# Optimization experiments

Hardware: AMD Instinct MI355X
Metric: run time of the kernel (lower is better)

## Reference

```python
import jax, jax.numpy as jnp
import numpy as np

SEQ_LEN = 512; PATCH = 16; STRIDE = 8; D_MODEL = 768; N_HEAD = 12; N_LAYERS = 6
POOL = 1000; TOP_K = 4; PRED_LEN = 96; TREND_W = 24; SEAS = 24
PATCH_NUM = (SEQ_LEN - PATCH) // STRIDE + 2  # 64, incl. the replication-padded patch
B = 64; M = 7


def _ln(x, g, b, eps=1e-5):
    mu = jnp.mean(x, axis=-1, keepdims=True)
    v = jnp.var(x, axis=-1, keepdims=True)
    return (x - mu) * jax.lax.rsqrt(v + eps) * g + b


def _decompose(x):
    # x: [N, L]. pandas: rolling(TREND_W, center=True).mean() + bfill/ffill,
    # then seasonal = groupby(index % SEAS).transform('mean') of detrended.
    N, L = x.shape
    w = TREND_W
    right = (w - 1) // 2          # pandas centered window: [i - (w-1-right), i + right]
    left = w - 1 - right
    cs = jnp.concatenate([jnp.zeros((N, 1), x.dtype), jnp.cumsum(x, axis=1)], axis=1)
    valid = (cs[:, w:] - cs[:, :-w]) / w                      # [N, L-w+1]
    trend = jnp.concatenate([jnp.repeat(valid[:, :1], left, axis=1), valid,
                             jnp.repeat(valid[:, -1:], right, axis=1)], axis=1)
    det = x - trend
    ids = jnp.arange(L) % SEAS
    onehot = jax.nn.one_hot(ids, SEAS, dtype=x.dtype)         # [L, S]
    gmean = (det @ onehot) / jnp.sum(onehot, axis=0)          # [N, S]
    seasonal = gmean[:, ids]
    resid = x - trend - seasonal
    return jnp.stack([trend, seasonal, resid], axis=1)        # [N, 3, L]


def _gpt2(h, wpe, layer_params, lnf_g, lnf_b):
    Bh, T, D = h.shape
    h = h + wpe[:T]
    mask = jnp.tril(jnp.ones((T, T), bool))
    hd = D // N_HEAD

    def block(h, p):
        ln1g, ln1b, qkvw, qkvb, aw, ab, ln2g, ln2b, fcw, fcb, pw, pb = p
        a = _ln(h, ln1g, ln1b)
        qkv = a @ qkvw + qkvb
        q, k, v = jnp.split(qkv, 3, axis=-1)
        sh = lambda t: t.reshape(Bh, T, N_HEAD, hd).transpose(0, 2, 1, 3)
        q, k, v = sh(q), sh(k), sh(v)
        s = jnp.einsum('bhqd,bhkd->bhqk', q, k) / jnp.sqrt(jnp.asarray(hd, h.dtype))
        s = jnp.where(mask, s, jnp.asarray(-1e9, h.dtype))
        att = jax.nn.softmax(s, axis=-1)
        o = jnp.einsum('bhqk,bhkd->bhqd', att, v).transpose(0, 2, 1, 3).reshape(Bh, T, D)
        h = h + o @ aw + ab
        m = _ln(h, ln2g, ln2b)
        h = h + jax.nn.gelu(m @ fcw + fcb, approximate=True) @ pw + pb
        return h, None

    h, _ = jax.lax.scan(block, h, layer_params)
    return _ln(h, lnf_g, lnf_b)


def setup_inputs() -> dict:
    key = jax.random.key(0)
    ks = jax.random.split(key, 10)
    D = D_MODEL; F = 4 * D
    f32 = jnp.float32
    return dict(
        x=jax.random.normal(ks[0], (B, SEQ_LEN, M), f32),
        itr=1,
        in_w=jax.random.normal(ks[1], (3 * PATCH, D), f32) * 0.02,
        in_b=jnp.zeros((D,), f32),
        prompt_key=jax.random.uniform(ks[2], (POOL, D), f32, -1.0, 1.0),
        wpe=jax.random.normal(ks[3], (1024, D), f32) * 0.02,
        ln1_g=jnp.ones((N_LAYERS, D), f32), ln1_b=jnp.zeros((N_LAYERS, D), f32),
        qkv_w=jax.random.normal(ks[4], (N_LAYERS, D, 3 * D), f32) * 0.02,
        qkv_b=jnp.zeros((N_LAYERS, 3 * D), f32),
        aproj_w=jax.random.normal(ks[5], (N_LAYERS, D, D), f32) * 0.02,
        aproj_b=jnp.zeros((N_LAYERS, D), f32),
        ln2_g=jnp.ones((N_LAYERS, D), f32), ln2_b=jnp.zeros((N_LAYERS, D), f32),
        fc_w=jax.random.normal(ks[6], (N_LAYERS, D, F), f32) * 0.02,
        fc_b=jnp.zeros((N_LAYERS, F), f32),
        mproj_w=jax.random.normal(ks[7], (N_LAYERS, F, D), f32) * 0.02,
        mproj_b=jnp.zeros((N_LAYERS, D), f32),
        lnf_g=jnp.ones((D,), f32), lnf_b=jnp.zeros((D,), f32),
        out_w=jax.random.normal(ks[8], ((D // 3) * (PATCH_NUM + TOP_K), PRED_LEN), f32) * 0.02,
        out_b=jnp.zeros((PRED_LEN,), f32),
    )


def reference(x, itr, in_w, in_b, prompt_key, wpe, ln1_g, ln1_b, qkv_w, qkv_b,
              aproj_w, aproj_b, ln2_g, ln2_b, fc_w, fc_b, mproj_w, mproj_b,
              lnf_g, lnf_b, out_w, out_b):
    B_, L, M_ = x.shape
    means = jax.lax.stop_gradient(jnp.mean(x, axis=1, keepdims=True))     # detached
    xc = x - means
    stdev = jax.lax.stop_gradient(jnp.sqrt(jnp.var(xc, axis=1, keepdims=True) + 1e-5))
    xn = xc / stdev
    xr = jnp.transpose(xn, (0, 2, 1)).reshape(B_ * M_, L)                  # 'b l m -> (b m) l'
    dec = jax.lax.stop_gradient(_decompose(xr))                            # torch detaches via numpy round-trip
    # ReplicationPad1d((0, STRIDE)) then unfold(size=PATCH, step=STRIDE)
    xpad = jnp.concatenate([dec, jnp.repeat(dec[:, :, -1:], STRIDE, axis=2)], axis=2)
    starts = jnp.arange(PATCH_NUM) * STRIDE
    patches = xpad[:, :, starts[:, None] + jnp.arange(PATCH)[None, :]]     # [BM, 3, N, P]
    tok = jnp.transpose(patches, (0, 2, 1, 3)).reshape(B_ * M_, PATCH_NUM, 3 * PATCH)
    emb = tok @ in_w + in_b                                                # [BM, N, D]
    # prompt-pool retrieval (L2P-style, length=1, prompts = normalized keys)
    l2n = lambda t: t * jax.lax.rsqrt(jnp.maximum(jnp.sum(t * t, -1, keepdims=True), 1e-12))
    key_n = l2n(prompt_key)                                                # [POOL, D]
    xq = l2n(jnp.mean(emb, axis=1))                                        # [BM, D]
    sim = xq @ key_n.T                                                     # [BM, POOL]
    _, idx = jax.lax.top_k(sim, TOP_K)
    bp = key_n[idx]                                                        # [BM, K, D]
    reduce_sim = jnp.sum(bp * xq[:, None, :]) / emb.shape[0]
    prompted = jnp.concatenate([bp, emb], axis=1)                          # [BM, K+N, D]
    layer_params = (ln1_g, ln1_b, qkv_w, qkv_b, aproj_w, aproj_b,
                    ln2_g, ln2_b, fc_w, fc_b, mproj_w, mproj_b)
    h = _gpt2(prompted, wpe, layer_params, lnf_g, lnf_b)                   # [BM, K+N, D]
    o = h.reshape(B_ * M_ * 3, -1) @ out_w + out_b                         # [BM*3, PRED_LEN]
    o = o.reshape(B_, M_, 3, PRED_LEN).sum(axis=2)                         # [B, M, H]
    out = jnp.transpose(o, (0, 2, 1)) * stdev + means                      # [B, H, M]
    return out, reduce_sim
```

## Files before the change

### kernel.cpp

```cpp
#include <hip/hip_runtime.h>
#include <math.h>

#define NTOK 30464
#define NEMB 28672
typedef unsigned short ushort;
typedef __attribute__((ext_vector_type(8))) __bf16 bf16x8_t;
typedef __attribute__((ext_vector_type(4))) float f32x4_t;

#if defined(__has_builtin)
#if __has_builtin(__builtin_amdgcn_global_load_lds)
#define HAS_GLL 1
#endif
#endif

__device__ __forceinline__ ushort f2bf(float f) {
  unsigned int u = __float_as_uint(f);
  u += 0x7fffu + ((u >> 16) & 1u);
  return (ushort)(u >> 16);
}
__device__ __forceinline__ float bf2f(ushort u) {
  return __uint_as_float(((unsigned int)u) << 16);
}

#ifdef HAS_GLL
__device__ __forceinline__ void gll16(const ushort* g, ushort* l) {
  __builtin_amdgcn_global_load_lds(
      (const __attribute__((address_space(1))) unsigned int*)g,
      (__attribute__((address_space(3))) unsigned int*)l, 16, 0, 0);
}
#endif

__device__ __forceinline__ float block_reduce_sum(float v, float* scratch) {
  __syncthreads();
  #pragma unroll
  for (int o = 32; o; o >>= 1) v += __shfl_xor(v, o, 64);
  int wid = threadIdx.x >> 6, lane = threadIdx.x & 63;
  if (lane == 0) scratch[wid] = v;
  __syncthreads();
  if (threadIdx.x == 0) {
    float s = 0.f;
    int nw = (blockDim.x + 63) >> 6;
    for (int i = 0; i < nw; i++) s += scratch[i];
    scratch[0] = s;
  }
  __syncthreads();
  return scratch[0];
}

__device__ __forceinline__ float gelu_f(float x) {
  float z2 = 1.5957691216057308f * (x + 0.044715f * x * x * x);
  return x / (1.0f + __expf(-z2));
}

__global__ __launch_bounds__(256) void revin_kernel(const float* __restrict__ x,
    float* __restrict__ xr, float* __restrict__ means, float* __restrict__ stdev) {
  int bm = blockIdx.x;
  int b = bm / 7, m = bm % 7;
  int tid = threadIdx.x;
  __shared__ float red[8];
  float v0 = x[(size_t)b * 3584 + (size_t)tid * 7 + m];
  float v1 = x[(size_t)b * 3584 + (size_t)(tid + 256) * 7 + m];
  float s  = block_reduce_sum(v0 + v1, red);
  float ss = block_reduce_sum(v0 * v0 + v1 * v1, red);
  float mean = s * (1.0f / 512.0f);
  float var  = ss * (1.0f / 512.0f) - mean * mean;
  float sd = sqrtf(var + 1e-5f);
  if (tid == 0) { means[bm] = mean; stdev[bm] = sd; }
  float inv = 1.0f / sd;
  xr[(size_t)bm * 512 + tid]       = (v0 - mean) * inv;
  xr[(size_t)bm * 512 + tid + 256] = (v1 - mean) * inv;
}

__global__ __launch_bounds__(256) void decompose_kernel(const float* __restrict__ xr,
    float* __restrict__ dec) {
  int n = blockIdx.x, tid = threadIdx.x;
  __shared__ float xv[512];
  __shared__ float tr[512];
  __shared__ float sumS[24];
  for (int l = tid; l < 512; l += 256) xv[l] = xr[(size_t)n * 512 + l];
  if (tid < 24) sumS[tid] = 0.f;
  __syncthreads();
  for (int l = tid; l < 512; l += 256) {
    int t0 = l - 12; t0 = t0 < 0 ? 0 : (t0 > 488 ? 488 : t0);
    float s = 0.f;
    #pragma unroll
    for (int j = 0; j < 24; j++) s += xv[t0 + j];
    float t = s * (1.0f / 24.0f);
    tr[l] = t;
    atomicAdd(&sumS[l % 24], xv[l] - t);
  }
  __syncthreads();
  if (tid < 24) sumS[tid] *= (tid < 8) ? (1.0f / 22.0f) : (1.0f / 21.0f);
  __syncthreads();
  float* dp = dec + (size_t)n * 1536;
  for (int l = tid; l < 512; l += 256) {
    float t = tr[l], se = sumS[l % 24];
    dp[l] = t;
    dp[512 + l] = se;
    dp[1024 + l] = xv[l] - t - se;
  }
}

__global__ __launch_bounds__(256) void embed_kernel(const float* __restrict__ dec,
    const float* __restrict__ in_w, const float* __restrict__ in_b, float* __restrict__ h) {
  int blk = blockIdx.x;
  int n = blk >> 2, pg = blk & 3;
  int tid = threadIdx.x;
  __shared__ __align__(16) float tok[16][48];
  for (int idx = tid; idx < 768; idx += 256) {
    int p = idx / 48, k = idx - p * 48;
    int c = k >> 4, j = k & 15;
    int l = (pg * 16 + p) * 8 + j; if (l > 511) l = 511;
    tok[p][k] = dec[(size_t)n * 1536 + (size_t)c * 512 + l];
  }
  __syncthreads();
  const int d0 = tid, d1 = tid + 256, d2 = tid + 512;
  float acc[16][3];
  float b0 = in_b[d0], b1 = in_b[d1], b2 = in_b[d2];
  #pragma unroll
  for (int p = 0; p < 16; p++) { acc[p][0] = b0; acc[p][1] = b1; acc[p][2] = b2; }
  for (int kq = 0; kq < 12; kq++) {
    float w0[4], w1[4], w2[4];
    #pragma unroll
    for (int kk = 0; kk < 4; kk++) {
      const float* wp = in_w + (size_t)(kq * 4 + kk) * 768;
      w0[kk] = wp[d0]; w1[kk] = wp[d1]; w2[kk] = wp[d2];
    }
    #pragma unroll
    for (int p = 0; p < 16; p++) {
      float4 t = *(const float4*)&tok[p][kq * 4];
      acc[p][0] += t.x * w0[0]; acc[p][1] += t.x * w1[0]; acc[p][2] += t.x * w2[0];
      acc[p][0] += t.y * w0[1]; acc[p][1] += t.y * w1[1]; acc[p][2] += t.y * w2[1];
      acc[p][0] += t.z * w0[2]; acc[p][1] += t.z * w1[2]; acc[p][2] += t.z * w2[2];
      acc[p][0] += t.w * w0[3]; acc[p][1] += t.w * w1[3]; acc[p][2] += t.w * w2[3];
    }
  }
  #pragma unroll
  for (int p = 0; p < 16; p++) {
    float* outp = h + ((size_t)n * 68 + 4 + pg * 16 + p) * 768;
    outp[d0] = acc[p][0]; outp[d1] = acc[p][1]; outp[d2] = acc[p][2];
  }
}

__global__ __launch_bounds__(256) void keyn_kernel(const float* __restrict__ pkey,
    float* __restrict__ keyn, double* __restrict__ kinv) {
  int k = blockIdx.x, tid = threadIdx.x;
  __shared__ double redd[4];
  float v[3];
  double ss = 0.0;
  #pragma unroll
  for (int i = 0; i < 3; i++) {
    v[i] = pkey[(size_t)k * 768 + tid + i * 256];
    ss += (double)v[i] * (double)v[i];
  }
  #pragma unroll
  for (int o = 32; o; o >>= 1) ss += __shfl_xor(ss, o, 64);
  int wid = tid >> 6, lane = tid & 63;
  if (lane == 0) redd[wid] = ss;
  __syncthreads();
  if (tid == 0) redd[0] = redd[0] + redd[1] + redd[2] + redd[3];
  __syncthreads();
  ss = redd[0];
  double inv = 1.0 / sqrt(ss > 1e-12 ? ss : 1e-12);
  #pragma unroll
  for (int i = 0; i < 3; i++)
    keyn[(size_t)k * 768 + tid + i * 256] = (float)((double)v[i] * inv);
  if (tid == 0) kinv[k] = inv;
}

__global__ __launch_bounds__(256) void xq_kernel(const float* __restrict__ h,
    float* __restrict__ xq) {
  int n = blockIdx.x, tid = threadIdx.x;
  __shared__ float red[8];
  float vals[3];
  float ssl = 0.f;
  #pragma unroll
  for (int i = 0; i < 3; i++) {
    int d = tid + i * 256;
    const float* p = h + ((size_t)n * 68 + 4) * 768 + d;
    float s = 0.f;
    for (int pc = 0; pc < 64; pc++) s += p[(size_t)pc * 768];
    s *= (1.0f / 64.0f);
    vals[i] = s; ssl += s * s;
  }
  float ss = block_reduce_sum(ssl, red);
  float inv = rsqrtf(fmaxf(ss, 1e-12f));
  #pragma unroll
  for (int i = 0; i < 3; i++)
    xq[(size_t)n * 768 + tid + i * 256] = vals[i] * inv;
}

__global__ void zero_kernel(float* p) {
  if (threadIdx.x == 0 && blockIdx.x == 0) p[0] = 0.f;
}

__global__ __launch_bounds__(256) void sim_kernel(
    const float* __restrict__ xq, const float* __restrict__ pkey,
    const double* __restrict__ kinv, double* __restrict__ simd) {
  int n = blockIdx.y;
  int kbase = blockIdx.x * 128;
  int tid = threadIdx.x;
  __shared__ __align__(16) float xqv[768];
  #pragma unroll
  for (int i = 0; i < 3; i++) xqv[tid + i * 256] = xq[(size_t)n * 768 + tid + i * 256];
  __syncthreads();
  int lane = tid & 63, wid = tid >> 6;
  double xd[12];
  #pragma unroll
  for (int i = 0; i < 12; i++) xd[i] = (double)xqv[lane * 12 + i];

  for (int k4 = kbase + wid * 4; k4 < kbase + 128; k4 += 16) {
    int kt[4];
    #pragma unroll
    for (int t = 0; t < 4; t++) { int k = k4 + t; kt[t] = k < 1000 ? k : 999; }
    float4 v[4][3];
    #pragma unroll
    for (int t = 0; t < 4; t++)
      #pragma unroll
      for (int j = 0; j < 3; j++)
        v[t][j] = *(const float4*)(pkey + (size_t)kt[t] * 768 + lane * 12 + j * 4);
    double a[4] = {0.0, 0.0, 0.0, 0.0};
    #pragma unroll
    for (int t = 0; t < 4; t++)
      #pragma unroll
      for (int j = 0; j < 3; j++) {
        a[t] += (double)v[t][j].x * xd[4 * j + 0];
        a[t] += (double)v[t][j].y * xd[4 * j + 1];
        a[t] += (double)v[t][j].z * xd[4 * j + 2];
        a[t] += (double)v[t][j].w * xd[4 * j + 3];
      }
    #pragma unroll
    for (int t = 0; t < 4; t++)
      #pragma unroll
      for (int o = 32; o; o >>= 1) a[t] += __shfl_xor(a[t], o, 64);
    if (lane == 0) {
      #pragma unroll
      for (int t = 0; t < 4; t++) {
        int k = k4 + t;
        if (k < 1000) simd[(size_t)n * 1000 + k] = a[t] * kinv[k];
      }
    }
  }
}

__global__ __launch_bounds__(256) void topk_kernel(
    const float* __restrict__ xq, const double* __restrict__ simd_g,
    const float* __restrict__ keyn, const float* __restrict__ wpe,
    float* __restrict__ h, float* __restrict__ rs_out) {
  int n = blockIdx.x, tid = threadIdx.x;
  __shared__ __align__(16) float xqv[768];
  __shared__ double simd_s[1000];
  __shared__ int idxs[4];
  __shared__ double redv[4];
  __shared__ int redi[4];
  __shared__ float red2[8];
  #pragma unroll
  for (int i = 0; i < 3; i++) xqv[tid + i * 256] = xq[(size_t)n * 768 + tid + i * 256];
  for (int k = tid; k < 1000; k += 256) simd_s[k] = simd_g[(size_t)n * 1000 + k];
  __syncthreads();
  int lane = tid & 63, wid = tid >> 6;
  for (int r = 0; r < 4; r++) {
    double bv = -1e300; int bi = 0x7fffffff;
    for (int k = tid; k < 1000; k += 256) {
      double v = simd_s[k];
      if (v > bv || (v == bv && k < bi)) { bv = v; bi = k; }
    }
    #pragma unroll
    for (int off = 32; off; off >>= 1) {
      double ov = __shfl_xor(bv, off, 64);
      int oi = __shfl_xor(bi, off, 64);
      if (ov > bv || (ov == bv && oi < bi)) { bv = ov; bi = oi; }
    }
    if (lane == 0) { redv[wid] = bv; redi[wid] = bi; }
    __syncthreads();
    if (tid == 0) {
      double fv = redv[0]; int fi = redi[0];
      for (int w = 1; w < 4; w++)
        if (redv[w] > fv || (redv[w] == fv && redi[w] < fi)) { fv = redv[w]; fi = redi[w]; }
      idxs[r] = fi; simd_s[fi] = -1e300;
    }
    __syncthreads();
  }
  float part = 0.f;
  for (int r = 0; r < 4; r++) {
    int ki = idxs[r];
    const float* kp = keyn + (size_t)ki * 768;
    const float* wp = wpe + (size_t)r * 768;
    float* hp = h + ((size_t)n * 68 + r) * 768;
    #pragma unroll
    for (int i = 0; i < 3; i++) {
      int d = tid + i * 256;
      float kv = kp[d];
      hp[d] = kv + wp[d];
      part += kv * xqv[d];
    }
  }
  part = block_reduce_sum(part, red2);
  if (tid == 0) atomicAdd(rs_out, part * (1.0f / 448.0f));
}

__global__ __launch_bounds__(256) void addwpe_kernel(const float* __restrict__ wpe,
    float* __restrict__ h) {
  int np = blockIdx.x;
  int n = np >> 6, p = np & 63;
  int tid = threadIdx.x;
  const float* wp = wpe + (size_t)(4 + p) * 768;
  float* hp = h + ((size_t)n * 68 + 4 + p) * 768;
  #pragma unroll
  for (int i = 0; i < 3; i++) { int d = tid + i * 256; hp[d] += wp[d]; }
}

__global__ __launch_bounds__(256) void ln_kernel(const float* __restrict__ src,
    ushort* __restrict__ dst, const float* __restrict__ g, const float* __restrict__ b) {
  size_t row = blockIdx.x;
  const float* xp = src + row * 768;
  ushort* yp = dst + row * 768;
  int tid = threadIdx.x;
  float v0 = xp[tid], v1 = xp[tid + 256], v2 = xp[tid + 512];
  __shared__ float red[8];
  float s  = block_reduce_sum(v0 + v1 + v2, red);
  float ss = block_reduce_sum(v0 * v0 + v1 * v1 + v2 * v2, red);
  float mean = s * (1.0f / 768.0f);
  float var  = ss * (1.0f / 768.0f) - mean * mean;
  float rs = rsqrtf(var + 1e-5f);
  yp[tid]       = f2bf((v0 - mean) * rs * g[tid]       + b[tid]);
  yp[tid + 256] = f2bf((v1 - mean) * rs * g[tid + 256] + b[tid + 256]);
  yp[tid + 512] = f2bf((v2 - mean) * rs * g[tid + 512] + b[tid + 512]);
}

__global__ __launch_bounds__(256) void tcast_kernel(const float* __restrict__ W,
    ushort* __restrict__ WT, int K, int N) {
  __shared__ ushort t[32][33];
  int n0 = blockIdx.x * 32, k0 = blockIdx.y * 32;
  int tx = threadIdx.x & 31, ty = threadIdx.x >> 5;
  #pragma unroll
  for (int i = 0; i < 4; i++) {
    int kk = ty + i * 8;
    t[kk][tx] = f2bf(W[(size_t)(k0 + kk) * N + n0 + tx]);
  }
  __syncthreads();
  #pragma unroll
  for (int i = 0; i < 4; i++) {
    int nn = ty + i * 8;
    WT[(size_t)(n0 + nn) * K + k0 + tx] = t[tx][nn];
  }
}

__global__ __launch_bounds__(256) void mfma_gemm(const ushort* __restrict__ A,
    const ushort* __restrict__ WT, const float* __restrict__ bias, void* __restrict__ Cp,
    int M, int N, int K, int mode) {
  __shared__ ushort As[128 * 32];
  __shared__ ushort Bs[128 * 32];
  const int tid = threadIdx.x;
  const int row0 = blockIdx.y * 128, col0 = blockIdx.x * 128;
  const int w = tid >> 6, lane = tid & 63;
  const int wm = w >> 1, wn = w & 1;
  const int lm = lane & 15, quad = lane >> 4;
  const int srow = w * 16 + (lane >> 2);
  const int scol = (lane & 3) * 8;
  const ushort* agp0 = A  + (size_t)(row0 + srow)      * K + scol;
  const ushort* agp1 = A  + (size_t)(row0 + 64 + srow) * K + scol;
  const ushort* bgp0 = WT + (size_t)(col0 + srow)      * K + scol;
  const ushort* bgp1 = WT + (size_t)(col0 + 64 + srow) * K + scol;
  ushort* al0 = &As[w * 512];
  ushort* al1 = &As[2048 + w * 512];
  ushort* bl0 = &Bs[w * 512];
  ushort* bl1 = &Bs[2048 + w * 512];
  f32x4_t acc[4][4];
  #pragma unroll
  for (int mi = 0; mi < 4; mi++)
    #pragma unroll
    for (int ni = 0; ni < 4; ni++) acc[mi][ni] = (f32x4_t)(0.0f);

  for (int kb = 0; kb < K; kb += 32) {
    __syncthreads();
#ifdef HAS_GLL
    gll16(agp0 + kb, al0);
    gll16(agp1 + kb, al1);
    gll16(bgp0 + kb, bl0);
    gll16(bgp1 + kb, bl1);
#else
    {
      uint4 va0 = *(const uint4*)(agp0 + kb);
      uint4 va1 = *(const uint4*)(agp1 + kb);
      uint4 vb0 = *(const uint4*)(bgp0 + kb);
      uint4 vb1 = *(const uint4*)(bgp1 + kb);
      *(uint4*)&al0[lane * 8] = va0;
      *(uint4*)&al1[lane * 8] = va1;
      *(uint4*)&bl0[lane * 8] = vb0;
      *(uint4*)&bl1[lane * 8] = vb1;
    }
#endif
    __syncthreads();
    bf16x8_t af[4], bfr[4];
    #pragma unroll
    for (int mi = 0; mi < 4; mi++)
      af[mi] = *(const bf16x8_t*)&As[(wm * 64 + mi * 16 + lm) * 32 + quad * 8];
    #pragma unroll
    for (int ni = 0; ni < 4; ni++)
      bfr[ni] = *(const bf16x8_t*)&Bs[(wn * 64 + ni * 16 + lm) * 32 + quad * 8];
    #pragma unroll
    for (int mi = 0; mi < 4; mi++)
      #pragma unroll
      for (int ni = 0; ni < 4; ni++)
        acc[mi][ni] = __builtin_amdgcn_mfma_f32_16x16x32_bf16(af[mi], bfr[ni], acc[mi][ni], 0, 0, 0);
  }
  #pragma unroll
  for (int mi = 0; mi < 4; mi++) {
    #pragma unroll
    for (int ni = 0; ni < 4; ni++) {
      int gcol = col0 + wn * 64 + ni * 16 + lm;
      float bz = bias[gcol];
      #pragma unroll
      for (int r = 0; r < 4; r++) {
        int grow = row0 + wm * 64 + mi * 16 + quad * 4 + r;
        float v = acc[mi][ni][r] + bz;
        if (mode == 0)      ((ushort*)Cp)[(size_t)grow * N + gcol] = f2bf(v);
        else if (mode == 1) ((ushort*)Cp)[(size_t)grow * N + gcol] = f2bf(gelu_f(v));
        else { float* c = (float*)Cp + (size_t)grow * N + gcol; *c += v; }
      }
    }
  }
}

__global__ __launch_bounds__(256) void attn_kernel(const ushort* __restrict__ qkvc,
    ushort* __restrict__ obase) {
  __shared__ __align__(16) ushort qk[2 * 80 * 64];
  __shared__ __align__(16) ushort vt[64][96];
  __shared__ __align__(16) float  sS[68][80];
  ushort* qs = qk;
  ushort* ks = qk + 80 * 64;
  ushort (*P)[96] = (ushort(*)[96])qk;

  int nh = blockIdx.x;
  int nl = nh / 12, hh = nh % 12;
  int tid = threadIdx.x;
  const int w = tid >> 6, lane = tid & 63;
  const int lm = lane & 15, quad = lane >> 4;
  const ushort* base = qkvc + (size_t)nl * 68 * 2304 + hh * 64;

  for (int idx = tid; idx < 68 * 64; idx += 256) {
    int t = idx >> 6, d = idx & 63;
    const ushort* rp = base + (size_t)t * 2304 + d;
    qs[t * 64 + d] = rp[0];
    ks[t * 64 + d] = rp[768];
    vt[d][t] = rp[1536];
  }
  for (int idx = tid; idx < 64 * 28; idx += 256) {
    int d = idx / 28, t = 68 + idx % 28;
    vt[d][t] = 0;
  }
  __syncthreads();

  for (int t5 = w; t5 < 25; t5 += 4) {
    int mi = t5 / 5, ni = t5 % 5;
    bf16x8_t a0 = *(const bf16x8_t*)&qs[(mi * 16 + lm) * 64 + quad * 8];
    bf16x8_t a1 = *(const bf16x8_t*)&qs[(mi * 16 + lm) * 64 + 32 + quad * 8];
    bf16x8_t b0 = *(const bf16x8_t*)&ks[(ni * 16 + lm) * 64 + quad * 8];
    bf16x8_t b1 = *(const bf16x8_t*)&ks[(ni * 16 + lm) * 64 + 32 + quad * 8];
    f32x4_t acc = (f32x4_t)(0.0f);
    acc = __builtin_amdgcn_mfma_f32_16x16x32_bf16(a0, b0, acc, 0, 0, 0);
    acc = __builtin_amdgcn_mfma_f32_16x16x32_bf16(a1, b1, acc, 0, 0, 0);
    int col = ni * 16 + lm;
    #pragma unroll
    for (int r = 0; r < 4; r++) {
      int row = mi * 16 + quad * 4 + r;
      if (row < 68) {
        float sv = (col > row || col >= 68) ? -1e9f : acc[r] * 0.125f;
        sS[row][col] = sv;
      }
    }
  }
  __syncthreads();

  if (tid < 68) {
    int r = tid;
    float mx = -1e30f;
    for (int c = 0; c < 80; c++) mx = fmaxf(mx, sS[r][c]);
    float sum = 0.f;
    for (int c = 0; c < 80; c++) { float e = __expf(sS[r][c] - mx); sS[r][c] = e; sum += e; }
    float inv = 1.0f / sum;
    for (int c = 0; c < 80; c++) P[r][c] = f2bf(sS[r][c] * inv);
    #pragma unroll
    for (int c = 80; c < 96; c++) P[r][c] = 0;
  } else if (tid < 80) {
    for (int c = 0; c < 96; c++) P[tid][c] = 0;
  }
  __syncthreads();

  for (int t5 = w; t5 < 20; t5 += 4) {
    int mi = t5 % 5, ni = t5 / 5;
    f32x4_t acc = (f32x4_t)(0.0f);
    #pragma unroll
    for (int kk = 0; kk < 3; kk++) {
      bf16x8_t a = *(const bf16x8_t*)&P[mi * 16 + lm][kk * 32 + quad * 8];
      bf16x8_t b = *(const bf16x8_t*)&vt[ni * 16 + lm][kk * 32 + quad * 8];
      acc = __builtin_amdgcn_mfma_f32_16x16x32_bf16(a, b, acc, 0, 0, 0);
    }
    int col = ni * 16 + lm;
    #pragma unroll
    for (int r = 0; r < 4; r++) {
      int row = mi * 16 + quad * 4 + r;
      if (row < 68)
        obase[((size_t)nl * 68 + row) * 768 + hh * 64 + col] = f2bf(acc[r]);
    }
  }
}

__global__ __launch_bounds__(256) void initof_kernel(const float* __restrict__ ob,
    float* __restrict__ of) {
  int i = blockIdx.x * 256 + threadIdx.x;
  of[i] = ob[i % 96];
}

__global__ __launch_bounds__(256) void splitk_kernel(const ushort* __restrict__ A,
    const ushort* __restrict__ WT, float* __restrict__ of) {
  __shared__ ushort As[64 * 32];
  __shared__ ushort Ws[96 * 32];
  const int tid = threadIdx.x;
  const int row0 = blockIdx.x * 64;
  const int k0 = blockIdx.y * 1024;
  const int w = tid >> 6, lane = tid & 63;
  const int lm = lane & 15, quad = lane >> 4;
  const ushort* agp  = A  + (size_t)(row0 + (tid >> 2)) * 17408 + (tid & 3) * 8;
  const ushort* wgp1 = WT + (size_t)(tid >> 2) * 17408 + (tid & 3) * 8;
  const ushort* wgp2 = WT + (size_t)(64 + (tid >> 2)) * 17408 + (tid & 3) * 8;
  ushort* asl  = &As[w * 512];
  ushort* wsl1 = &Ws[w * 512];
  ushort* wsl2 = &Ws[2048 + w * 512];
  f32x4_t acc[6];
  #pragma unroll
  for (int ni = 0; ni < 6; ni++) acc[ni] = (f32x4_t)(0.0f);
  for (int kb = k0; kb < k0 + 1024; kb += 32) {
    __syncthreads();
#ifdef HAS_GLL
    gll16(agp + kb, asl);
    gll16(wgp1 + kb, wsl1);
    if (w < 2) gll16(wgp2 + kb, wsl2);
#else
    {
      uint4 va = *(const uint4*)(agp + kb);
      *(uint4*)&As[tid * 8] = va;
      uint4 vw = *(const uint4*)(wgp1 + kb);
      *(uint4*)&Ws[tid * 8] = vw;
      if (tid < 128) {
        uint4 vw2 = *(const uint4*)(wgp2 + kb);
        *(uint4*)&Ws[2048 + tid * 8] = vw2;
      }
    }
#endif
    __syncthreads();
    bf16x8_t af = *(const bf16x8_t*)&As[(w * 16 + lm) * 32 + quad * 8];
    #pragma unroll
    for (int ni = 0; ni < 6; ni++) {
      bf16x8_t bfrag = *(const bf16x8_t*)&Ws[(ni * 16 + lm) * 32 + quad * 8];
      acc[ni] = __builtin_amdgcn_mfma_f32_16x16x32_bf16(af, bfrag, acc[ni], 0, 0, 0);
    }
  }
  #pragma unroll
  for (int ni = 0; ni < 6; ni++) {
    int col = ni * 16 + lm;
    #pragma unroll
    for (int r = 0; r < 4; r++) {
      int grow = row0 + w * 16 + quad * 4 + r;
      atomicAdd(&of[(size_t)grow * 96 + col], acc[ni][r]);
    }
  }
}

__global__ void combine_kernel(const float* __restrict__ of, const float* __restrict__ stdev,
    const float* __restrict__ means, float* __restrict__ out) {
  int bm = blockIdx.x;
  int b = bm / 7, m = bm % 7;
  int j = threadIdx.x;
  if (j < 96) {
    float s = of[(size_t)(bm * 3 + 0) * 96 + j]
            + of[(size_t)(bm * 3 + 1) * 96 + j]
            + of[(size_t)(bm * 3 + 2) * 96 + j];
    out[(size_t)b * 672 + (size_t)j * 7 + m] = s * stdev[bm] + means[bm];
  }
}

extern "C" void kernel_launch(void* const* d_in, const int* in_sizes, int n_in,
                              void* d_out, int out_size, void* d_ws, size_t ws_size,
                              hipStream_t stream) {
  (void)in_sizes; (void)n_in; (void)out_size;
  const float* x     = (const float*)d_in[0];
  const float* in_w  = (const float*)d_in[2];
  const float* in_b  = (const float*)d_in[3];
  const float* pkey  = (const float*)d_in[4];
  const float* wpe   = (const float*)d_in[5];
  const float* ln1_g = (const float*)d_in[6];
  const float* ln1_b = (const float*)d_in[7];
  const float* qkv_w = (const float*)d_in[8];
  const float* qkv_b = (const float*)d_in[9];
  const float* aw    = (const float*)d_in[10];
  const float* ab    = (const float*)d_in[11];
  const float* ln2_g = (const float*)d_in[12];
  const float* ln2_b = (const float*)d_in[13];
  const float* fc_w  = (const float*)d_in[14];
  const float* fc_b  = (const float*)d_in[15];
  const float* mp_w  = (const float*)d_in[16];
  const float* mp_b  = (const float*)d_in[17];
  const float* lnf_g = (const float*)d_in[18];
  const float* lnf_b = (const float*)d_in[19];
  const float* out_w = (const float*)d_in[20];
  const float* out_b = (const float*)d_in[21];
  float* out = (float*)d_out;
  float* ws  = (float*)d_ws;

  float* means = ws;
  float* stdev = ws + 512;
  float* xr    = ws + 1024;
  float* dec   = xr + 229376;
  float* keyn  = dec + 688128;
  double* kinv = (double*)(keyn + 768000);
  float* xq    = keyn + 768000 + 2048;
  float* of    = xq + 344064;
  float* h     = of + 129024;
  ushort* abuf16 = (ushort*)(h + 23396352);
  ushort* w16    = abuf16 + 23396352;
  ushort* scr16  = w16 + 7077888;
  ushort* owT16  = scr16;

  double* simd = (double*)xr;

  ushort* wqT  = w16;
  ushort* waT  = wqT + 2304 * 768;
  ushort* wfcT = waT + 768 * 768;
  ushort* wmpT = wfcT + 3072 * 768;

  size_t scr_bytes = ws_size - (size_t)((char*)scr16 - (char*)ws);
  long cap_qg = (long)(scr_bytes / (17ull * 128 * 2304 * 2));
  if (cap_qg > 14) cap_qg = 14;
  if (cap_qg < 1) cap_qg = 1;
  int nch_q = (int)((14 + cap_qg - 1) / cap_qg);
  int gpc = (14 + nch_q - 1) / nch_q;
  long cap_ft = (long)(scr_bytes / (128ull * 3072 * 2));
  if (cap_ft > 238) cap_ft = 238;
  if (cap_ft < 1) cap_ft = 1;
  int nch_f = (int)((238 + cap_ft - 1) / cap_ft);
  int tpc = (238 + nch_f - 1) / nch_f;

  revin_kernel<<<448, 256, 0, stream>>>(x, xr, means, stdev);
  decompose_kernel<<<448, 256, 0, stream>>>(xr, dec);
  embed_kernel<<<1792, 256, 0, stream>>>(dec, in_w, in_b, h);
  keyn_kernel<<<1000, 256, 0, stream>>>(pkey, keyn, kinv);
  xq_kernel<<<448, 256, 0, stream>>>(h, xq);
  zero_kernel<<<1, 64, 0, stream>>>(out + 43008);
  sim_kernel<<<dim3(8, 448), 256, 0, stream>>>(xq, pkey, kinv, simd);
  topk_kernel<<<448, 256, 0, stream>>>(xq, simd, keyn, wpe, h, out + 43008);
  addwpe_kernel<<<NEMB, 256, 0, stream>>>(wpe, h);

  for (int l = 0; l < 6; l++) {
    tcast_kernel<<<dim3(72, 24), 256, 0, stream>>>(qkv_w + (size_t)l * 768 * 2304, wqT, 768, 2304);
    tcast_kernel<<<dim3(24, 24), 256, 0, stream>>>(aw    + (size_t)l * 768 * 768,  waT, 768, 768);
    tcast_kernel<<<dim3(96, 24), 256, 0, stream>>>(fc_w  + (size_t)l * 768 * 3072, wfcT, 768, 3072);
    tcast_kernel<<<dim3(24, 96), 256, 0, stream>>>(mp_w  + (size_t)l * 3072 * 768, wmpT, 3072, 768);

    ln_kernel<<<NTOK, 256, 0, stream>>>(h, abuf16, ln1_g + l * 768, ln1_b + l * 768);
    for (int g0 = 0; g0 < 14; ) {
      int g = (gpc < 14 - g0) ? gpc : (14 - g0);
      int tiles = g * 17, rows = g * 2176, series = g * 32;
      ushort* Ain = abuf16 + (size_t)g0 * 2176 * 768;
      mfma_gemm<<<dim3(18, tiles), 256, 0, stream>>>(
          Ain, wqT, qkv_b + l * 2304, scr16, rows, 2304, 768, 0);
      attn_kernel<<<series * 12, 256, 0, stream>>>(scr16, Ain);
      g0 += g;
    }
    mfma_gemm<<<dim3(6, 238), 256, 0, stream>>>(
        abuf16, waT, ab + l * 768, h, NTOK, 768, 768, 2);
    ln_kernel<<<NTOK, 256, 0, stream>>>(h, abuf16, ln2_g + l * 768, ln2_b + l * 768);
    for (int t0 = 0; t0 < 238; ) {
      int t = (tpc < 238 - t0) ? tpc : (238 - t0);
      mfma_gemm<<<dim3(24, t), 256, 0, stream>>>(
          abuf16 + (size_t)t0 * 128 * 768, wfcT, fc_b + l * 3072, scr16,
          t * 128, 3072, 768, 1);
      mfma_gemm<<<dim3(6, t), 256, 0, stream>>>(
          scr16, wmpT, mp_b + l * 768, h + (size_t)t0 * 128 * 768,
          t * 128, 768, 3072, 2);
      t0 += t;
    }
  }
  ln_kernel<<<NTOK, 256, 0, stream>>>(h, abuf16, lnf_g, lnf_b);
  tcast_kernel<<<dim3(3, 544), 256, 0, stream>>>(out_w, owT16, 17408, 96);
  initof_kernel<<<504, 256, 0, stream>>>(out_b, of);
  splitk_kernel<<<dim3(21, 17), 256, 0, stream>>>(abuf16, owT16, of);
  combine_kernel<<<448, 96, 0, stream>>>(of, stdev, means, out);
}
```

Before: 6.622 ms.

## Replace 128x128 MFMA GEMM with double-buffered 256x256 eight-wave pipelined kernel

Swaps the single-buffered 128x128 bf16 GEMM for a 256x256-tile kernel with 512 threads that double-buffers K=64 slabs in LDS. Global-to-LDS loads for the next slab are issued between MFMA phases, with explicit vmcnt waits, barriers and setprio to overlap memory with compute. Chunk sizes are now rounded to even tile counts, and row bounds checks are added because M may not be a multiple of 256. The larger tile reduces global and LDS traffic per FLOP, at the cost of fewer blocks, 128KB of LDS per block and higher register pressure, which may limit occupancy.

```diff
diff --git a/kernel.cpp b/kernel.cpp
--- a/kernel.cpp
+++ b/kernel.cpp
@@ -346,78 +346,166 @@
   }
 }
 
-__global__ __launch_bounds__(256) void mfma_gemm(const ushort* __restrict__ A,
+__global__ __launch_bounds__(512, 2) void mfma_gemm256(const ushort* __restrict__ A,
     const ushort* __restrict__ WT, const float* __restrict__ bias, void* __restrict__ Cp,
     int M, int N, int K, int mode) {
-  __shared__ ushort As[128 * 32];
-  __shared__ ushort Bs[128 * 32];
+  __shared__ __align__(16) ushort lds[65536];
   const int tid = threadIdx.x;
-  const int row0 = blockIdx.y * 128, col0 = blockIdx.x * 128;
   const int w = tid >> 6, lane = tid & 63;
-  const int wm = w >> 1, wn = w & 1;
+  const int wm = w >> 2, wn = w & 3;
   const int lm = lane & 15, quad = lane >> 4;
-  const int srow = w * 16 + (lane >> 2);
-  const int scol = (lane & 3) * 8;
-  const ushort* agp0 = A  + (size_t)(row0 + srow)      * K + scol;
-  const ushort* agp1 = A  + (size_t)(row0 + 64 + srow) * K + scol;
-  const ushort* bgp0 = WT + (size_t)(col0 + srow)      * K + scol;
-  const ushort* bgp1 = WT + (size_t)(col0 + 64 + srow) * K + scol;
-  ushort* al0 = &As[w * 512];
-  ushort* al1 = &As[2048 + w * 512];
-  ushort* bl0 = &Bs[w * 512];
-  ushort* bl1 = &Bs[2048 + w * 512];
-  f32x4_t acc[4][4];
-  #pragma unroll
-  for (int mi = 0; mi < 4; mi++)
-    #pragma unroll
-    for (int ni = 0; ni < 4; ni++) acc[mi][ni] = (f32x4_t)(0.0f);
-
-  for (int kb = 0; kb < K; kb += 32) {
-    __syncthreads();
+  const int row0 = blockIdx.y * 256, col0 = blockIdx.x * 256;
+  const int nt = K >> 6;
+
+  const ushort* Asrc = A  + (size_t)(row0 + w * 16 + lm) * K + quad * 8;
+  const ushort* Bsrc = WT + (size_t)(col0 + w * 16 + lm) * K + quad * 8;
+  const size_t halfstep = (size_t)128 * K;
+  ushort* Adst = &lds[w * 1024];
+  ushort* Bdst = &lds[32768 + w * 1024];
+
 #ifdef HAS_GLL
-    gll16(agp0 + kb, al0);
-    gll16(agp1 + kb, al1);
-    gll16(bgp0 + kb, bl0);
-    gll16(bgp1 + kb, bl1);
+#define ISSUE_A(buf, hf, kb) do { \
+    gll16(Asrc + (size_t)(hf) * halfstep + (kb),      Adst + (buf) * 16384 + (hf) * 8192); \
+    gll16(Asrc + (size_t)(hf) * halfstep + (kb) + 32, Adst + (buf) * 16384 + (hf) * 8192 + 512); \
+  } while (0)
+#define ISSUE_B(buf, hf, kb) do { \
+    gll16(Bsrc + (size_t)(hf) * halfstep + (kb),      Bdst + (buf) * 16384 + (hf) * 8192); \
+    gll16(Bsrc + (size_t)(hf) * halfstep + (kb) + 32, Bdst + (buf) * 16384 + (hf) * 8192 + 512); \
+  } while (0)
+#define WAIT_VM4 asm volatile("s_waitcnt vmcnt(4)" ::: "memory")
+#define WAIT_VM0 asm volatile("s_waitcnt vmcnt(0)" ::: "memory")
 #else
-    {
-      uint4 va0 = *(const uint4*)(agp0 + kb);
-      uint4 va1 = *(const uint4*)(agp1 + kb);
-      uint4 vb0 = *(const uint4*)(bgp0 + kb);
-      uint4 vb1 = *(const uint4*)(bgp1 + kb);
-      *(uint4*)&al0[lane * 8] = va0;
-      *(uint4*)&al1[lane * 8] = va1;
-      *(uint4*)&bl0[lane * 8] = vb0;
-      *(uint4*)&bl1[lane * 8] = vb1;
-    }
+#define ISSUE_A(buf, hf, kb) do { \
+    uint4 v0 = *(const uint4*)(Asrc + (size_t)(hf) * halfstep + (kb)); \
+    uint4 v1 = *(const uint4*)(Asrc + (size_t)(hf) * halfstep + (kb) + 32); \
+    *(uint4*)&(Adst + (buf) * 16384 + (hf) * 8192)[lane * 8] = v0; \
+    *(uint4*)&(Adst + (buf) * 16384 + (hf) * 8192 + 512)[lane * 8] = v1; \
+  } while (0)
+#define ISSUE_B(buf, hf, kb) do { \
+    uint4 v0 = *(const uint4*)(Bsrc + (size_t)(hf) * halfstep + (kb)); \
+    uint4 v1 = *(const uint4*)(Bsrc + (size_t)(hf) * halfstep + (kb) + 32); \
+    *(uint4*)&(Bdst + (buf) * 16384 + (hf) * 8192)[lane * 8] = v0; \
+    *(uint4*)&(Bdst + (buf) * 16384 + (hf) * 8192 + 512)[lane * 8] = v1; \
+  } while (0)
+#define WAIT_VM4 asm volatile("s_waitcnt vmcnt(0) lgkmcnt(0)" ::: "memory")
+#define WAIT_VM0 asm volatile("s_waitcnt vmcnt(0) lgkmcnt(0)" ::: "memory")
 #endif
-    __syncthreads();
-    bf16x8_t af[4], bfr[4];
+
+  f32x4_t acc[8][4];
+  #pragma unroll
+  for (int mi = 0; mi < 8; mi++)
+    #pragma unroll
+    for (int nj = 0; nj < 4; nj++) acc[mi][nj] = (f32x4_t)(0.0f);
+
+  ISSUE_A(0, 0, 0); ISSUE_A(0, 1, 0);
+  ISSUE_B(0, 0, 0); ISSUE_B(0, 1, 0);
+  if (nt > 1) { ISSUE_A(1, 0, 64); ISSUE_A(1, 1, 64); WAIT_VM4; }
+  else       { WAIT_VM0; }
+  __builtin_amdgcn_sched_barrier(0);
+  __builtin_amdgcn_s_barrier();
+  __builtin_amdgcn_sched_barrier(0);
+
+  bf16x8_t af[4][2], bf0[2][2], bf1[2][2];
+  const int Abase = wm * 8192;
+  const int Bbase = 32768 + wn * 4096;
+
+  for (int t = 0; t < nt; ++t) {
+    const int c = (t & 1) * 16384;
+    const int kb = t * 64;
     #pragma unroll
     for (int mi = 0; mi < 4; mi++)
-      af[mi] = *(const bf16x8_t*)&As[(wm * 64 + mi * 16 + lm) * 32 + quad * 8];
-    #pragma unroll
-    for (int ni = 0; ni < 4; ni++)
-      bfr[ni] = *(const bf16x8_t*)&Bs[(wn * 64 + ni * 16 + lm) * 32 + quad * 8];
+      #pragma unroll
+      for (int ks = 0; ks < 2; ks++)
+        af[mi][ks] = *(const bf16x8_t*)&lds[c + Abase + mi * 1024 + ks * 512 + lane * 8];
+    #pragma unroll
+    for (int nj = 0; nj < 2; nj++)
+      #pragma unroll
+      for (int ks = 0; ks < 2; ks++)
+        bf0[nj][ks] = *(const bf16x8_t*)&lds[c + Bbase + nj * 1024 + ks * 512 + lane * 8];
+    if (t + 1 < nt) ISSUE_B(((t + 1) & 1), 0, kb + 64);
+    __builtin_amdgcn_s_setprio(1);
     #pragma unroll
     for (int mi = 0; mi < 4; mi++)
       #pragma unroll
-      for (int ni = 0; ni < 4; ni++)
-        acc[mi][ni] = __builtin_amdgcn_mfma_f32_16x16x32_bf16(af[mi], bfr[ni], acc[mi][ni], 0, 0, 0);
-  }
-  #pragma unroll
-  for (int mi = 0; mi < 4; mi++) {
-    #pragma unroll
-    for (int ni = 0; ni < 4; ni++) {
-      int gcol = col0 + wn * 64 + ni * 16 + lm;
+      for (int nj = 0; nj < 2; nj++)
+        #pragma unroll
+        for (int ks = 0; ks < 2; ks++)
+          acc[mi][nj] = __builtin_amdgcn_mfma_f32_16x16x32_bf16(af[mi][ks], bf0[nj][ks], acc[mi][nj], 0, 0, 0);
+    __builtin_amdgcn_s_setprio(0);
+    __builtin_amdgcn_sched_barrier(0);
+    __builtin_amdgcn_s_barrier();
+    __builtin_amdgcn_sched_barrier(0);
+    #pragma unroll
+    for (int nj = 0; nj < 2; nj++)
+      #pragma unroll
+      for (int ks = 0; ks < 2; ks++)
+        bf1[nj][ks] = *(const bf16x8_t*)&lds[c + Bbase + (2 + nj) * 1024 + ks * 512 + lane * 8];
+    if (t + 1 < nt) ISSUE_B(((t + 1) & 1), 1, kb + 64);
+    __builtin_amdgcn_s_setprio(1);
+    #pragma unroll
+    for (int mi = 0; mi < 4; mi++)
+      #pragma unroll
+      for (int nj = 0; nj < 2; nj++)
+        #pragma unroll
+        for (int ks = 0; ks < 2; ks++)
+          acc[mi][2 + nj] = __builtin_amdgcn_mfma_f32_16x16x32_bf16(af[mi][ks], bf1[nj][ks], acc[mi][2 + nj], 0, 0, 0);
+    __builtin_amdgcn_s_setprio(0);
+    __builtin_amdgcn_sched_barrier(0);
+    __builtin_amdgcn_s_barrier();
+    __builtin_amdgcn_sched_barrier(0);
+    #pragma unroll
+    for (int mi = 0; mi < 4; mi++)
+      #pragma unroll
+      for (int ks = 0; ks < 2; ks++)
+        af[mi][ks] = *(const bf16x8_t*)&lds[c + Abase + (4 + mi) * 1024 + ks * 512 + lane * 8];
+    __builtin_amdgcn_s_setprio(1);
+    #pragma unroll
+    for (int mi = 0; mi < 4; mi++)
+      #pragma unroll
+      for (int nj = 0; nj < 2; nj++)
+        #pragma unroll
+        for (int ks = 0; ks < 2; ks++)
+          acc[4 + mi][2 + nj] = __builtin_amdgcn_mfma_f32_16x16x32_bf16(af[mi][ks], bf1[nj][ks], acc[4 + mi][2 + nj], 0, 0, 0);
+    __builtin_amdgcn_s_setprio(0);
+    __builtin_amdgcn_sched_barrier(0);
+    __builtin_amdgcn_s_barrier();
+    __builtin_amdgcn_sched_barrier(0);
+    if (t + 2 < nt) { ISSUE_A((t & 1), 0, kb + 128); ISSUE_A((t & 1), 1, kb + 128); }
+    __builtin_amdgcn_s_setprio(1);
+    #pragma unroll
+    for (int mi = 0; mi < 4; mi++)
+      #pragma unroll
+      for (int nj = 0; nj < 2; nj++)
+        #pragma unroll
+        for (int ks = 0; ks < 2; ks++)
+          acc[4 + mi][nj] = __builtin_amdgcn_mfma_f32_16x16x32_bf16(af[mi][ks], bf0[nj][ks], acc[4 + mi][nj], 0, 0, 0);
+    __builtin_amdgcn_s_setprio(0);
+    if (t + 2 < nt) { WAIT_VM4; }
+    else if (t + 1 < nt) { WAIT_VM0; }
+    __builtin_amdgcn_sched_barrier(0);
+    if (t + 1 < nt) { __builtin_amdgcn_s_barrier(); __builtin_amdgcn_sched_barrier(0); }
+  }
+
+#undef ISSUE_A
+#undef ISSUE_B
+#undef WAIT_VM4
+#undef WAIT_VM0
+
+  #pragma unroll
+  for (int mi = 0; mi < 8; mi++) {
+    #pragma unroll
+    for (int nj = 0; nj < 4; nj++) {
+      int gcol = col0 + wn * 64 + nj * 16 + lm;
       float bz = bias[gcol];
       #pragma unroll
       for (int r = 0; r < 4; r++) {
-        int grow = row0 + wm * 64 + mi * 16 + quad * 4 + r;
-        float v = acc[mi][ni][r] + bz;
-        if (mode == 0)      ((ushort*)Cp)[(size_t)grow * N + gcol] = f2bf(v);
-        else if (mode == 1) ((ushort*)Cp)[(size_t)grow * N + gcol] = f2bf(gelu_f(v));
-        else { float* c = (float*)Cp + (size_t)grow * N + gcol; *c += v; }
+        int grow = row0 + wm * 128 + mi * 16 + quad * 4 + r;
+        if (grow < M) {
+          float v = acc[mi][nj][r] + bz;
+          if (mode == 0)      ((ushort*)Cp)[(size_t)grow * N + gcol] = f2bf(v);
+          else if (mode == 1) ((ushort*)Cp)[(size_t)grow * N + gcol] = f2bf(gelu_f(v));
+          else { float* cc = (float*)Cp + (size_t)grow * N + gcol; *cc += v; }
+        }
       }
     }
   }
@@ -634,13 +722,13 @@
   long cap_qg = (long)(scr_bytes / (17ull * 128 * 2304 * 2));
   if (cap_qg > 14) cap_qg = 14;
   if (cap_qg < 1) cap_qg = 1;
-  int nch_q = (int)((14 + cap_qg - 1) / cap_qg);
-  int gpc = (14 + nch_q - 1) / nch_q;
+  int gpc = (int)cap_qg;
+  if (gpc > 1) gpc &= ~1;
   long cap_ft = (long)(scr_bytes / (128ull * 3072 * 2));
   if (cap_ft > 238) cap_ft = 238;
   if (cap_ft < 1) cap_ft = 1;
-  int nch_f = (int)((238 + cap_ft - 1) / cap_ft);
-  int tpc = (238 + nch_f - 1) / nch_f;
+  int tpc = (int)cap_ft;
+  if (tpc > 1) tpc &= ~1;
 
   revin_kernel<<<448, 256, 0, stream>>>(x, xr, means, stdev);
   decompose_kernel<<<448, 256, 0, stream>>>(xr, dec);
@@ -661,24 +749,25 @@
     ln_kernel<<<NTOK, 256, 0, stream>>>(h, abuf16, ln1_g + l * 768, ln1_b + l * 768);
     for (int g0 = 0; g0 < 14; ) {
       int g = (gpc < 14 - g0) ? gpc : (14 - g0);
-      int tiles = g * 17, rows = g * 2176, series = g * 32;
+      int rows = g * 2176, series = g * 32;
       ushort* Ain = abuf16 + (size_t)g0 * 2176 * 768;
-      mfma_gemm<<<dim3(18, tiles), 256, 0, stream>>>(
+      mfma_gemm256<<<dim3(9, (rows + 255) / 256), 512, 0, stream>>>(
           Ain, wqT, qkv_b + l * 2304, scr16, rows, 2304, 768, 0);
       attn_kernel<<<series * 12, 256, 0, stream>>>(scr16, Ain);
       g0 += g;
     }
-    mfma_gemm<<<dim3(6, 238), 256, 0, stream>>>(
+    mfma_gemm256<<<dim3(3, 119), 512, 0, stream>>>(
         abuf16, waT, ab + l * 768, h, NTOK, 768, 768, 2);
     ln_kernel<<<NTOK, 256, 0, stream>>>(h, abuf16, ln2_g + l * 768, ln2_b + l * 768);
     for (int t0 = 0; t0 < 238; ) {
       int t = (tpc < 238 - t0) ? tpc : (238 - t0);
-      mfma_gemm<<<dim3(24, t), 256, 0, stream>>>(
+      int rows = t * 128;
+      mfma_gemm256<<<dim3(12, (rows + 255) / 256), 512, 0, stream>>>(
           abuf16 + (size_t)t0 * 128 * 768, wfcT, fc_b + l * 3072, scr16,
-          t * 128, 3072, 768, 1);
-      mfma_gemm<<<dim3(6, t), 256, 0, stream>>>(
+          rows, 3072, 768, 1);
+      mfma_gemm256<<<dim3(3, (rows + 255) / 256), 512, 0, stream>>>(
           scr16, wmpT, mp_b + l * 768, h + (size_t)t0 * 128 * 768,
-          t * 128, 768, 3072, 2);
+          rows, 768, 3072, 2);
       t0 += t;
     }
   }
```

Result: slower. 8.013 ms (+21.0%).
